# Kernel tuning notes

Hardware: AMD Instinct MI355X
Metric: run time of the kernel (lower is better)

The kernel has to match this reference:

```python
import jax, jax.numpy as jnp
import numpy as np

B, N, C = 16, 3136, 576
HEADS, AG, WIN, PS = 8, 49, 56, 7


def setup_inputs() -> dict:
    key = jax.random.key(0)
    ks = jax.random.split(key, 14)
    std = 0.02
    d = {
        "x": jax.random.normal(ks[0], (B, N, C), jnp.float32),
        "Wq": std * jax.random.normal(ks[1], (C, C), jnp.float32),
        "Wkv": std * jax.random.normal(ks[2], (C, 2 * C), jnp.float32),
        "an_bias": std * jax.random.normal(ks[3], (HEADS, AG, 7, 7), jnp.float32),
        "na_bias": std * jax.random.normal(ks[4], (HEADS, AG, 7, 7), jnp.float32),
        "ah_bias": std * jax.random.normal(ks[5], (1, HEADS, AG, WIN, 1), jnp.float32),
        "aw_bias": std * jax.random.normal(ks[6], (1, HEADS, AG, 1, WIN), jnp.float32),
        "ha_bias": std * jax.random.normal(ks[7], (1, HEADS, WIN, 1, AG), jnp.float32),
        "wa_bias": std * jax.random.normal(ks[8], (1, HEADS, 1, WIN, AG), jnp.float32),
        "dwc_w": std * jax.random.normal(ks[9], (C, 1, 3, 3), jnp.float32),  # depthwise 3x3
        "dwc_gamma": jnp.ones((C,), jnp.float32),
        "dwc_beta": jnp.zeros((C,), jnp.float32),
        "proj_w": std * jax.random.normal(ks[10], (C, C), jnp.float32),
        "proj_b": jnp.zeros((C,), jnp.float32),
        "H": 56,
        "W": 56,
    }
    return d


def _forward(x, Wq, Wkv, an_bias, na_bias, ah_bias, aw_bias, ha_bias, wa_bias,
             dwc_w, dwc_gamma, dwc_beta, proj_w, proj_b, H, W):
    b, n, c = x.shape
    heads, ag = an_bias.shape[0], an_bias.shape[1]
    hd = c // heads
    scale = hd ** -0.5

    q = x @ Wq                     # [b, n, c]
    kv = x @ Wkv                   # [b, n, 2c]
    k, v = kv[..., :c], kv[..., c:]

    # agent tokens: adaptive avg pool q (H,W grid) down to (PS, PS)
    ps = int(round(ag ** 0.5))
    qa = q.reshape(b, ps, H // ps, ps, W // ps, c).mean(axis=(2, 4))  # [b, ps, ps, c]
    a = qa.reshape(b, ag, heads, hd).transpose(0, 2, 1, 3)            # [b, h, ag, hd]

    qh = q.reshape(b, n, heads, hd).transpose(0, 2, 1, 3)  # [b, h, n, hd]
    kh = k.reshape(b, n, heads, hd).transpose(0, 2, 1, 3)
    vh = v.reshape(b, n, heads, hd).transpose(0, 2, 1, 3)

    # stage 1: agent attends to K/V, with interpolated + separable position bias
    pb1 = jax.image.resize(an_bias, (heads, ag, H, W), "linear").reshape(1, heads, ag, n)
    pb2 = (ah_bias + aw_bias).reshape(1, heads, ag, n)
    agent_scores = jnp.einsum("bhad,bhnd->bhan", a * scale, kh) + pb1 + pb2
    agent_attn = jax.nn.softmax(agent_scores, axis=-1)
    agent_v = jnp.einsum("bhan,bhnd->bhad", agent_attn, vh)  # [b, h, ag, hd]

    # stage 2: queries attend to agent tokens
    ab1 = jax.image.resize(na_bias, (heads, ag, H, W), "linear").reshape(1, heads, ag, n)
    ab1 = ab1.transpose(0, 1, 3, 2)                                   # [1, h, n, ag]
    ab2 = (ha_bias + wa_bias).reshape(1, heads, n, ag)
    q_scores = jnp.einsum("bhnd,bhad->bhna", qh * scale, a) + ab1 + ab2
    q_attn = jax.nn.softmax(q_scores, axis=-1)
    out = jnp.einsum("bhna,bhad->bhnd", q_attn, agent_v)
    out = out.transpose(0, 2, 1, 3).reshape(b, n, c)

    # depthwise-conv branch on v (DW_bn_relu, BN in eval mode with unit stats)
    vimg = v.transpose(0, 2, 1).reshape(b, c, H, W)
    y = jax.lax.conv_general_dilated(vimg, dwc_w, (1, 1), "SAME",
                                     feature_group_count=c,
                                     dimension_numbers=("NCHW", "OIHW", "NCHW"))
    y = jax.nn.relu(y * dwc_gamma[None, :, None, None] + dwc_beta[None, :, None, None])
    y = y.reshape(b, c, n).transpose(0, 2, 1)

    out = out + y
    out = out @ proj_w + proj_b   # output projection
    return out


def reference(x, Wq, Wkv, an_bias, na_bias, ah_bias, aw_bias, ha_bias, wa_bias,
              dwc_w, dwc_gamma, dwc_beta, proj_w, proj_b, H, W):
    return _forward(x, Wq, Wkv, an_bias, na_bias, ah_bias, aw_bias, ha_bias, wa_bias,
                    dwc_w, dwc_gamma, dwc_beta, proj_w, proj_b, H, W)
```

## Files before the change

kernel.cpp:

```cpp
#include <hip/hip_runtime.h>
#include <stdint.h>

typedef unsigned short u16;
typedef u16   u16x4 __attribute__((ext_vector_type(4)));
typedef u16   u16x8 __attribute__((ext_vector_type(8)));
typedef float f32x4 __attribute__((ext_vector_type(4)));
typedef __bf16 bf16x8 __attribute__((ext_vector_type(8)));

#define BB    16
#define NN    3136
#define CC    576
#define HEADS 8
#define HD    72
#define AGN   49
#define NTOT  1728
#define NCH   6
#define SCALE 0.1178511301977579f

__device__ __forceinline__ u16 f2bf(float f) {
    unsigned u = __float_as_uint(f);
    return (u16)((u + 0x7fffu + ((u >> 16) & 1u)) >> 16);
}
__device__ __forceinline__ float bf2f(u16 u) {
    return __uint_as_float(((unsigned)u) << 16);
}

__global__ __launch_bounds__(256) void k_cast_x(const float* __restrict__ x, u16* __restrict__ xb) {
    size_t i = (size_t)blockIdx.x * 256 + threadIdx.x;
    f32x4 v = *(const f32x4*)(x + i * 4);
    u16x4 o; o[0] = f2bf(v[0]); o[1] = f2bf(v[1]); o[2] = f2bf(v[2]); o[3] = f2bf(v[3]);
    *(u16x4*)(xb + i * 4) = o;
}

__global__ __launch_bounds__(256) void k_prep_w(const float* __restrict__ Wq, const float* __restrict__ Wkv,
                                                const float* __restrict__ Wp,
                                                u16* __restrict__ wbT, u16* __restrict__ wpT) {
    int idx = blockIdx.x * 256 + threadIdx.x;
    if (idx < NTOT * CC) {
        int nn = idx / CC, kk = idx % CC;
        float v = (nn < CC) ? Wq[kk * CC + nn] : Wkv[kk * (2 * CC) + (nn - CC)];
        wbT[idx] = f2bf(v);
    } else {
        int j = idx - NTOT * CC;
        int nn = j / CC, kk = j % CC;
        wpT[j] = f2bf(Wp[kk * CC + nn]);
    }
}

__device__ __forceinline__ float bilerp7(const float* __restrict__ g, int oy, int ox) {
    float cy = (oy - 3.5f) * 0.125f;
    float cx = (ox - 3.5f) * 0.125f;
    float fy0 = floorf(cy), fx0 = floorf(cx);
    float ty = cy - fy0, tx = cx - fx0;
    int iy0 = (int)fy0, ix0 = (int)fx0;
    int y0 = min(6, max(0, iy0)), y1 = min(6, max(0, iy0 + 1));
    int x0 = min(6, max(0, ix0)), x1 = min(6, max(0, ix0 + 1));
    float g00 = g[y0 * 7 + x0], g01 = g[y0 * 7 + x1];
    float g10 = g[y1 * 7 + x0], g11 = g[y1 * 7 + x1];
    return (1.f - ty) * ((1.f - tx) * g00 + tx * g01) + ty * ((1.f - tx) * g10 + tx * g11);
}

__global__ __launch_bounds__(256) void k_bias1(const float* __restrict__ an, const float* __restrict__ ah,
                                               const float* __restrict__ aw, float* __restrict__ b1) {
    int idx = blockIdx.x * 256 + threadIdx.x;
    int ag = idx % AGN; int r = idx / AGN; int n = r % NN; int h = r / NN;
    int y = n / 56, x = n % 56;
    float v = bilerp7(an + (h * AGN + ag) * 49, y, x);
    b1[idx] = v + ah[(h * AGN + ag) * 56 + y] + aw[(h * AGN + ag) * 56 + x];
}

__global__ __launch_bounds__(256) void k_bias2(const float* __restrict__ na, const float* __restrict__ ha,
                                               const float* __restrict__ wa, float* __restrict__ b2p) {
    int idx = blockIdx.x * 256 + threadIdx.x;
    int ag = idx & 63; int r = idx >> 6; int n = r % NN; int h = r / NN;
    float v;
    if (ag < AGN) {
        int y = n / 56, x = n % 56;
        v = bilerp7(na + (h * AGN + ag) * 49, y, x)
          + ha[(h * 56 + y) * AGN + ag] + wa[(h * 56 + x) * AGN + ag];
    } else v = -1e30f;
    b2p[idx] = v;
}

template<int MODE>
__global__ __launch_bounds__(256) void k_gemm(const u16* __restrict__ A, const u16* __restrict__ Bt,
                                              u16* __restrict__ Qp, u16* __restrict__ Kp, u16* __restrict__ Vp,
                                              float* __restrict__ Cf, const float* __restrict__ bias,
                                              const int M) {
    const int NB = (MODE == 0) ? NTOT : CC;
    __shared__ u16 SMEM[2 * 128 * 64];
    u16* Asm = SMEM;
    u16* Bsm = SMEM + 128 * 64;
    const int t = threadIdx.x, lane = t & 63, wid = t >> 6;
    const int wm = wid & 1, wn = wid >> 1;
    const int nwg = gridDim.x * gridDim.y;
    const int id = blockIdx.y * gridDim.x + blockIdx.x;
    const int qq = nwg >> 3, rr = nwg & 7;
    const int xcd = id & 7, off = id >> 3;
    const int nid = (xcd < rr ? xcd * (qq + 1) : rr * (qq + 1) + (xcd - rr) * qq) + off;
    const int row0 = (nid / gridDim.x) * 128, col0 = (nid % gridDim.x) * 128;
    const int lr = lane & 15, lk = lane >> 4;
    f32x4 acc[4][4];
#pragma unroll
    for (int m = 0; m < 4; m++)
#pragma unroll
        for (int n2 = 0; n2 < 4; n2++) acc[m][n2] = (f32x4)0.f;

    for (int kt = 0; kt < 9; ++kt) {
        const int k0 = kt * 64;
#pragma unroll
        for (int it = 0; it < 4; ++it) {
            int flat = it * 256 + wid * 64 + lane;
            int r = flat >> 3, lc = (flat & 7) ^ (r & 7);
            int arow = min(row0 + r, M - 1);
            const u16* src = A + (size_t)arow * CC + k0 + lc * 8;
            __builtin_amdgcn_global_load_lds((const __attribute__((address_space(1))) void*)src,
                                             (__attribute__((address_space(3))) void*)(&Asm[(it * 256 + wid * 64) * 8]),
                                             16, 0, 0);
        }
#pragma unroll
        for (int it = 0; it < 4; ++it) {
            int flat = it * 256 + wid * 64 + lane;
            int r = flat >> 3, lc = (flat & 7) ^ (r & 7);
            int brow = min(col0 + r, NB - 1);
            const u16* src = Bt + (size_t)brow * CC + k0 + lc * 8;
            __builtin_amdgcn_global_load_lds((const __attribute__((address_space(1))) void*)src,
                                             (__attribute__((address_space(3))) void*)(&Bsm[(it * 256 + wid * 64) * 8]),
                                             16, 0, 0);
        }
        __syncthreads();
#pragma unroll
        for (int kk = 0; kk < 2; ++kk) {
            const int klocal2 = (kk * 32 + lk * 8) * 2;
            bf16x8 av[4], bv[4];
#pragma unroll
            for (int m = 0; m < 4; m++) {
                int row = wm * 64 + m * 16 + lr;
                av[m] = *(const bf16x8*)((const char*)Asm + row * 128 + (klocal2 ^ ((row & 7) << 4)));
            }
#pragma unroll
            for (int n2 = 0; n2 < 4; n2++) {
                int row = wn * 64 + n2 * 16 + lr;
                bv[n2] = *(const bf16x8*)((const char*)Bsm + row * 128 + (klocal2 ^ ((row & 7) << 4)));
            }
#pragma unroll
            for (int m = 0; m < 4; m++)
#pragma unroll
                for (int n2 = 0; n2 < 4; n2++)
                    acc[m][n2] = __builtin_amdgcn_mfma_f32_16x16x32_bf16(av[m], bv[n2], acc[m][n2], 0, 0, 0);
        }
        __syncthreads();
    }

    if (MODE == 0) {
#pragma unroll
        for (int n2 = 0; n2 < 4; n2++) {
            int cgl = col0 + wn * 64 + n2 * 16 + lr;
            if (cgl >= NB) continue;
            int which = cgl / 576;
            int rem = cgl - which * 576;
            int hh = rem / 72;
            int dd = rem - hh * 72;
            u16* dst = which == 0 ? Qp : (which == 1 ? Kp : Vp);
#pragma unroll
            for (int m = 0; m < 4; m++)
#pragma unroll
                for (int j = 0; j < 4; j++) {
                    int rgl = row0 + wm * 64 + m * 16 + lk * 4 + j;
                    int b = rgl / NN, n = rgl - b * NN;
                    dst[((size_t)(b * 8 + hh) * NN + n) * 72 + dd] = f2bf(acc[m][n2][j]);
                }
        }
    } else {
        float* Ef = (float*)SMEM;
#pragma unroll
        for (int ph = 0; ph < 4; ++ph) {
            if (wm == (ph >> 1)) {
#pragma unroll
                for (int mm = 0; mm < 2; mm++) {
                    int m = (ph & 1) * 2 + mm;
#pragma unroll
                    for (int n2 = 0; n2 < 4; n2++) {
                        int col = wn * 64 + n2 * 16 + lr;
                        float addv = (MODE == 1) ? bias[min(col0 + col, NB - 1)] : 0.f;
#pragma unroll
                        for (int j = 0; j < 4; j++)
                            Ef[(mm * 16 + lk * 4 + j) * 136 + col] = acc[m][n2][j] + addv;
                    }
                }
            }
            __syncthreads();
#pragma unroll
            for (int cc2 = 0; cc2 < 4; ++cc2) {
                int cidx = cc2 * 256 + t;
                int rl = cidx >> 5, colc = cidx & 31;
                int cgl = col0 + colc * 4;
                int rgl = row0 + ph * 32 + rl;
                if (cgl < NB && rgl < M) {
                    f32x4 v = *(const f32x4*)&Ef[rl * 136 + colc * 4];
                    *(f32x4*)(Cf + (size_t)rgl * 576 + cgl) = v;
                }
            }
            __syncthreads();
        }
    }
}

__global__ __launch_bounds__(256) void k_poolx(const u16* __restrict__ xb, u16* __restrict__ px) {
    const int t = threadIdx.x;
    const int b = blockIdx.x / 7, p1 = blockIdx.x % 7;
    for (int task = t; task < 504; task += 256) {
        int p2 = task / 72, c8 = task - p2 * 72;
        const u16* base = xb + ((size_t)b * NN + (p1 * 8) * 56 + p2 * 8) * CC + c8 * 8;
        float s[8] = {0.f, 0.f, 0.f, 0.f, 0.f, 0.f, 0.f, 0.f};
        for (int y = 0; y < 8; ++y)
#pragma unroll
            for (int x = 0; x < 8; ++x) {
                u16x8 v = *(const u16x8*)(base + (size_t)(y * 56 + x) * CC);
#pragma unroll
                for (int j = 0; j < 8; j++) s[j] += bf2f(v[j]);
            }
        u16x8 o;
#pragma unroll
        for (int j = 0; j < 8; j++) o[j] = f2bf(s[j] * 0.015625f);
        *(u16x8*)(px + (size_t)(b * AGN + p1 * 7 + p2) * CC + c8 * 8) = o;
    }
}

__global__ __launch_bounds__(256) void k_stageA(const u16* __restrict__ Kp, const u16* __restrict__ Vp,
                                                const float* __restrict__ a_f, const float* __restrict__ b1,
                                                float* __restrict__ part) {
    const int t = threadIdx.x, lane = t & 63, w = t >> 6;
    const int c = lane & 15, g = lane >> 4;
    const int bh = blockIdx.y, b = bh >> 3, h = bh & 7;
    const int chunk = blockIdx.x;
    const int t0 = (chunk == 0) ? 0 : 9 + 8 * (chunk - 1);
    const int ntile = (chunk == 0) ? 9 : 8;

    __shared__ u16 A_lds[64][104];
    __shared__ u16 K_lds[64][104];
    __shared__ u16 Vt[80][72];
    __shared__ u16 P_lds[64][72];

    for (int i = t; i < 64 * 104; i += 256) {
        int r = i / 104, cc = i - r * 104;
        if (cc >= 72 || r >= 49) A_lds[r][cc] = 0;
        if (cc >= 72) K_lds[r][cc] = 0;
    }
    for (int i = t; i < 8 * 72; i += 256) Vt[72 + i / 72][i % 72] = 0;
    for (int i = t; i < 49 * 72; i += 256) {
        int r = i / 72, d = i - r * 72;
        A_lds[r][d] = f2bf(a_f[(size_t)(b * 49 + r) * CC + h * 72 + d] * SCALE);
    }
    __syncthreads();

    bf16x8 bfA[3];
#pragma unroll
    for (int ks = 0; ks < 3; ++ks) bfA[ks] = *(const bf16x8*)&A_lds[16 * w + c][8 * g + 32 * ks];

    float m_run = -1e30f, l_run = 0.f;
    f32x4 acc[5];
#pragma unroll
    for (int dt = 0; dt < 5; ++dt) acc[dt] = (f32x4)0.f;

    const u16* kb = Kp + ((size_t)(b * 8 + h) * NN + t0 * 64) * 72;
    const u16* vb = Vp + ((size_t)(b * 8 + h) * NN + t0 * 64) * 72;
    const int arow = min(16 * w + c, 48);

    for (int tile = 0; tile < ntile; ++tile) {
        for (int i = t; i < 576; i += 256) {
            int nl = i / 9, ch = i - nl * 9;
            u16x8 kd = *(const u16x8*)(kb + (size_t)tile * 4608 + i * 8);
            *(u16x8*)&K_lds[nl][ch * 8] = kd;
        }
        for (int i = t; i < 576; i += 256) {
            int ch = i >> 6, nl = i & 63;
            u16x8 vd = *(const u16x8*)(vb + (size_t)tile * 4608 + (nl * 9 + ch) * 8);
#pragma unroll
            for (int j = 0; j < 8; j++) Vt[ch * 8 + j][nl] = vd[j];
        }
        __syncthreads();

        f32x4 sT[4];
        const int nbase = (t0 + tile) * 64 + 4 * g;
#pragma unroll
        for (int nm = 0; nm < 4; ++nm) {
            f32x4 sv;
#pragma unroll
            for (int j = 0; j < 4; j++)
                sv[j] = b1[(size_t)(h * NN + nbase + 16 * nm + j) * AGN + arow];
#pragma unroll
            for (int ks = 0; ks < 3; ++ks) {
                bf16x8 af = *(const bf16x8*)&K_lds[16 * nm + c][8 * g + 32 * ks];
                sv = __builtin_amdgcn_mfma_f32_16x16x32_bf16(af, bfA[ks], sv, 0, 0, 0);
            }
            sT[nm] = sv;
        }

        float mt = sT[0][0];
#pragma unroll
        for (int nm = 0; nm < 4; ++nm)
#pragma unroll
            for (int j = 0; j < 4; j++) mt = fmaxf(mt, sT[nm][j]);
        mt = fmaxf(mt, __shfl_xor(mt, 16, 64));
        mt = fmaxf(mt, __shfl_xor(mt, 32, 64));
        float mnew = fmaxf(m_run, mt);
        float ps = 0.f;
#pragma unroll
        for (int nm = 0; nm < 4; ++nm) {
            float p0 = __expf(sT[nm][0] - mnew);
            float p1 = __expf(sT[nm][1] - mnew);
            float p2 = __expf(sT[nm][2] - mnew);
            float p3 = __expf(sT[nm][3] - mnew);
            ps += (p0 + p1) + (p2 + p3);
            unsigned pk01 = ((unsigned)f2bf(p1) << 16) | f2bf(p0);
            unsigned pk23 = ((unsigned)f2bf(p3) << 16) | f2bf(p2);
            unsigned* dst = (unsigned*)&P_lds[16 * w + c][16 * nm + 4 * g];
            dst[0] = pk01; dst[1] = pk23;
        }
        ps += __shfl_xor(ps, 16, 64);
        ps += __shfl_xor(ps, 32, 64);
        float rsc = __expf(m_run - mnew);
        l_run = l_run * rsc + ps;
        m_run = mnew;

        float rj[4];
#pragma unroll
        for (int j = 0; j < 4; j++) rj[j] = __shfl(rsc, 4 * g + j, 64);
        bf16x8 pa[2];
#pragma unroll
        for (int ks = 0; ks < 2; ++ks) pa[ks] = *(const bf16x8*)&P_lds[16 * w + c][8 * g + 32 * ks];
#pragma unroll
        for (int dt = 0; dt < 5; ++dt) {
            f32x4 a0 = acc[dt];
#pragma unroll
            for (int j = 0; j < 4; j++) a0[j] *= rj[j];
#pragma unroll
            for (int ks = 0; ks < 2; ++ks) {
                bf16x8 vf = *(const bf16x8*)&Vt[16 * dt + c][8 * g + 32 * ks];
                a0 = __builtin_amdgcn_mfma_f32_16x16x32_bf16(pa[ks], vf, a0, 0, 0, 0);
            }
            acc[dt] = a0;
        }
        __syncthreads();
    }

    const size_t pbase = (size_t)(bh * NCH + chunk) * (49 * 74);
#pragma unroll
    for (int dt = 0; dt < 5; ++dt) {
        int d = 16 * dt + c;
        if (d < 72) {
#pragma unroll
            for (int j = 0; j < 4; j++) {
                int agent = 16 * w + 4 * g + j;
                if (agent < 49) part[pbase + agent * 74 + d] = acc[dt][j];
            }
        }
    }
    if (g == 0) {
        int agent = 16 * w + c;
        if (agent < 49) {
            part[pbase + agent * 74 + 72] = m_run;
            part[pbase + agent * 74 + 73] = l_run;
        }
    }
}

__global__ __launch_bounds__(256) void k_reduceA(const float* __restrict__ part, float* __restrict__ agv) {
    const int bh = blockIdx.x, t = threadIdx.x;
    const float* pb = part + (size_t)bh * NCH * (49 * 74);
    for (int idx = t; idx < 49 * 72; idx += 256) {
        int row = idx / 72, d = idx - row * 72;
        float m = -1e30f;
#pragma unroll
        for (int c = 0; c < NCH; c++) m = fmaxf(m, pb[c * (49 * 74) + row * 74 + 72]);
        float accv = 0.f, l = 0.f;
#pragma unroll
        for (int c = 0; c < NCH; c++) {
            const float* pc = pb + c * (49 * 74) + row * 74;
            float e = __expf(pc[72] - m);
            accv += pc[d] * e;
            l += pc[73] * e;
        }
        agv[(size_t)(bh * 49 + row) * 72 + d] = accv / l;
    }
}

__global__ __launch_bounds__(256) void k_stageBC(const u16* __restrict__ Qp, const float* __restrict__ a_f,
                                                 const float* __restrict__ agv, const float* __restrict__ b2p,
                                                 const u16* __restrict__ Vp, const float* __restrict__ cw,
                                                 const float* __restrict__ gamma, const float* __restrict__ beta,
                                                 u16* __restrict__ pre) {
    const int t = threadIdx.x, lane = t & 63, w = t >> 6;
    const int c = lane & 15, g = lane >> 4;
    const int bh = blockIdx.y, b = bh >> 3, h = bh & 7;
    const int n0 = blockIdx.x * 256;

    __shared__ u16 A_lds[64][104];
    __shared__ u16 avT[80][72];
    __shared__ u16 Pt[4][64][80];
    __shared__ float wle[72 * 9];
    __shared__ float gle[72], ble[72];

    for (int i = t; i < 64 * 104; i += 256) {
        int r = i / 104, cc = i - r * 104;
        if (cc >= 72 || r >= 49) A_lds[r][cc] = 0;
    }
    for (int i = t; i < 80 * 72; i += 256) ((u16*)avT)[i] = 0;
    for (int i = t; i < 648; i += 256) wle[i] = cw[h * 648 + i];
    if (t < 72) { gle[t] = gamma[h * 72 + t]; ble[t] = beta[h * 72 + t]; }
    __syncthreads();
    for (int i = t; i < 49 * 72; i += 256) {
        int r = i / 72, d = i - r * 72;
        A_lds[r][d] = f2bf(a_f[(size_t)(b * 49 + r) * CC + h * 72 + d] * SCALE);
        avT[d][r]   = f2bf(agv[(size_t)(bh * 49 + r) * 72 + d]);
    }
    __syncthreads();

    bf16x8 afr[4][3];
#pragma unroll
    for (int mt = 0; mt < 4; ++mt)
#pragma unroll
        for (int ks = 0; ks < 3; ++ks) afr[mt][ks] = *(const bf16x8*)&A_lds[16 * mt + c][8 * g + 32 * ks];

    const int nw0 = n0 + w * 64;
#pragma unroll
    for (int cg = 0; cg < 4; ++cg) {
        const int n = nw0 + 16 * cg + c;
        const int ne = min(n, NN - 1);
        const u16* qp = Qp + ((size_t)(b * 8 + h) * NN + ne) * 72;
        bf16x8 qf[3];
#pragma unroll
        for (int ks = 0; ks < 3; ++ks) qf[ks] = *(const bf16x8*)(qp + 8 * g + 32 * ks);
        const float* bp = b2p + (size_t)(h * NN + ne) * 64;
        f32x4 sv[4];
#pragma unroll
        for (int mt = 0; mt < 4; ++mt) sv[mt] = *(const f32x4*)(bp + 16 * mt + 4 * g);
#pragma unroll
        for (int ks = 0; ks < 3; ++ks)
#pragma unroll
            for (int mt = 0; mt < 4; ++mt)
                sv[mt] = __builtin_amdgcn_mfma_f32_16x16x32_bf16(afr[mt][ks], qf[ks], sv[mt], 0, 0, 0);
        float mx = sv[0][0];
#pragma unroll
        for (int mt = 0; mt < 4; ++mt)
#pragma unroll
            for (int j = 0; j < 4; j++) mx = fmaxf(mx, sv[mt][j]);
        mx = fmaxf(mx, __shfl_xor(mx, 16, 64));
        mx = fmaxf(mx, __shfl_xor(mx, 32, 64));
        float ps = 0.f;
#pragma unroll
        for (int mt = 0; mt < 4; ++mt) {
#pragma unroll
            for (int j = 0; j < 4; j++) { sv[mt][j] = __expf(sv[mt][j] - mx); ps += sv[mt][j]; }
        }
        ps += __shfl_xor(ps, 16, 64);
        ps += __shfl_xor(ps, 32, 64);
        float inv = 1.f / ps;
#pragma unroll
        for (int mt = 0; mt < 4; ++mt) {
            unsigned pk01 = ((unsigned)f2bf(sv[mt][1] * inv) << 16) | f2bf(sv[mt][0] * inv);
            unsigned pk23 = ((unsigned)f2bf(sv[mt][3] * inv) << 16) | f2bf(sv[mt][2] * inv);
            unsigned* dst = (unsigned*)&Pt[w][16 * cg + c][16 * mt + 4 * g];
            dst[0] = pk01; dst[1] = pk23;
        }
    }
    bf16x8 vfr[5][2];
#pragma unroll
    for (int dt = 0; dt < 5; ++dt)
#pragma unroll
        for (int ks = 0; ks < 2; ++ks) vfr[dt][ks] = *(const bf16x8*)&avT[16 * dt + c][8 * g + 32 * ks];
#pragma unroll
    for (int rt = 0; rt < 4; ++rt) {
        bf16x8 pf[2];
#pragma unroll
        for (int ks = 0; ks < 2; ++ks) pf[ks] = *(const bf16x8*)&Pt[w][16 * rt + c][8 * g + 32 * ks];
#pragma unroll
        for (int dt = 0; dt < 5; ++dt) {
            f32x4 a0 = (f32x4)0.f;
            a0 = __builtin_amdgcn_mfma_f32_16x16x32_bf16(pf[0], vfr[dt][0], a0, 0, 0, 0);
            a0 = __builtin_amdgcn_mfma_f32_16x16x32_bf16(pf[1], vfr[dt][1], a0, 0, 0, 0);
            int dd = 16 * dt + c;
            if (dd < 72) {
#pragma unroll
                for (int j = 0; j < 4; j++)
                    Pt[w][16 * rt + 4 * g + j][dd] = f2bf(a0[j]);
            }
        }
    }
    __syncthreads();

    const u16* PtF = &Pt[0][0][0];
    const u16* vh = Vp + ((size_t)(b * 8 + h) * NN) * 72;
    for (int task = t; task < 256 * 9; task += 256) {
        int tl = task / 9, ch = task - tl * 9;
        int n = n0 + tl;
        if (n >= NN) continue;
        int y = n / 56, x = n % 56;
        float a[8] = {0.f, 0.f, 0.f, 0.f, 0.f, 0.f, 0.f, 0.f};
#pragma unroll
        for (int dy = -1; dy <= 1; ++dy) {
            int yy = y + dy; if (yy < 0 || yy > 55) continue;
#pragma unroll
            for (int dx = -1; dx <= 1; ++dx) {
                int xx = x + dx; if (xx < 0 || xx > 55) continue;
                u16x8 vv = *(const u16x8*)(vh + (size_t)(yy * 56 + xx) * 72 + ch * 8);
                int tap = (dy + 1) * 3 + (dx + 1);
#pragma unroll
                for (int j = 0; j < 8; j++) a[j] += bf2f(vv[j]) * wle[(ch * 8 + j) * 9 + tap];
            }
        }
        u16x8 ov = *(const u16x8*)&PtF[tl * 80 + ch * 8];
        u16x8 rr2;
#pragma unroll
        for (int j = 0; j < 8; j++)
            rr2[j] = f2bf(bf2f(ov[j]) + fmaxf(a[j] * gle[ch * 8 + j] + ble[ch * 8 + j], 0.f));
        *(u16x8*)(pre + ((size_t)b * NN + n) * CC + h * 72 + ch * 8) = rr2;
    }
}

extern "C" void kernel_launch(void* const* d_in, const int* in_sizes, int n_in,
                              void* d_out, int out_size, void* d_ws, size_t ws_size,
                              hipStream_t stream) {
    const float* x     = (const float*)d_in[0];
    const float* Wq    = (const float*)d_in[1];
    const float* Wkv   = (const float*)d_in[2];
    const float* an_b  = (const float*)d_in[3];
    const float* na_b  = (const float*)d_in[4];
    const float* ah_b  = (const float*)d_in[5];
    const float* aw_b  = (const float*)d_in[6];
    const float* ha_b  = (const float*)d_in[7];
    const float* wa_b  = (const float*)d_in[8];
    const float* dwcw  = (const float*)d_in[9];
    const float* gam   = (const float*)d_in[10];
    const float* bet   = (const float*)d_in[11];
    const float* projw = (const float*)d_in[12];
    const float* projb = (const float*)d_in[13];
    float* out = (float*)d_out;

    char* ws = (char*)d_ws;
    u16* wbT  = (u16*)(ws + 0);
    u16* wpT  = (u16*)(ws + 1990656);
    u16* xb   = (u16*)(ws + 2654208);
    u16* Qp   = (u16*)(ws + 60456960);
    u16* Kp   = (u16*)(ws + 118259712);
    u16* Vp   = (u16*)(ws + 176062464);
    float* af = (float*)(ws + 233865216);
    u16* px   = (u16*)(ws + 235671552);
    float* agv= (float*)(ws + 235671552);
    float* b1 = (float*)(ws + 237477888);
    float* b2p= (float*)(ws + 242395136);
    float* part = (float*)xb;

    k_cast_x<<<28224, 256, 0, stream>>>(x, xb);
    k_prep_w<<<5184, 256, 0, stream>>>(Wq, Wkv, projw, wbT, wpT);
    k_bias1<<<4802, 256, 0, stream>>>(an_b, ah_b, aw_b, b1);
    k_bias2<<<6272, 256, 0, stream>>>(na_b, ha_b, wa_b, b2p);
    k_poolx<<<112, 256, 0, stream>>>(xb, px);
    k_gemm<2><<<dim3(5, 7), 256, 0, stream>>>(px, wbT, nullptr, nullptr, nullptr, af, nullptr, 784);
    k_gemm<0><<<dim3(14, 392), 256, 0, stream>>>(xb, wbT, Qp, Kp, Vp, nullptr, nullptr, BB * NN);
    k_stageA<<<dim3(NCH, 128), 256, 0, stream>>>(Kp, Vp, af, b1, part);
    k_reduceA<<<128, 256, 0, stream>>>(part, agv);
    k_stageBC<<<dim3(13, 128), 256, 0, stream>>>(Qp, af, agv, b2p, Vp, dwcw, gam, bet, xb );
    k_gemm<1><<<dim3(5, 392), 256, 0, stream>>>(xb , wpT, nullptr, nullptr, nullptr, out, projb, BB * NN);
}
```

Before: 487.7 us.

## Precompute scaled agent and transposed agent-V bf16 tiles outside stageBC

Result: faster. 442.0 us (-9.4%).

```diff
diff --git a/kernel.cpp b/kernel.cpp
--- a/kernel.cpp
+++ b/kernel.cpp
@@ -227,6 +227,15 @@
     }
 }
 
+__global__ __launch_bounds__(256) void k_prepA(const float* __restrict__ a_f, u16* __restrict__ aSc) {
+    int idx = blockIdx.x * 256 + threadIdx.x;
+    int d = idx % 96; int r = (idx / 96) & 63; int bh = idx / (96 * 64);
+    int b = bh >> 3, h = bh & 7;
+    u16 v = 0;
+    if (r < AGN && d < HD) v = f2bf(a_f[((size_t)b * AGN + r) * CC + h * HD + d] * SCALE);
+    aSc[idx] = v;
+}
+
 __global__ __launch_bounds__(256) void k_stageA(const u16* __restrict__ Kp, const u16* __restrict__ Vp,
                                                 const float* __restrict__ a_f, const float* __restrict__ b1,
                                                 float* __restrict__ part) {
@@ -366,9 +375,12 @@
     }
 }
 
-__global__ __launch_bounds__(256) void k_reduceA(const float* __restrict__ part, float* __restrict__ agv) {
+__global__ __launch_bounds__(256) void k_reduceA(const float* __restrict__ part, u16* __restrict__ avTg) {
     const int bh = blockIdx.x, t = threadIdx.x;
     const float* pb = part + (size_t)bh * NCH * (49 * 74);
+    u16* av = avTg + (size_t)bh * 80 * 72;
+    for (int i = t; i < 80 * 72; i += 256) av[i] = 0;
+    __syncthreads();
     for (int idx = t; idx < 49 * 72; idx += 256) {
         int row = idx / 72, d = idx - row * 72;
         float m = -1e30f;
@@ -382,12 +394,12 @@
             accv += pc[d] * e;
             l += pc[73] * e;
         }
-        agv[(size_t)(bh * 49 + row) * 72 + d] = accv / l;
-    }
-}
-
-__global__ __launch_bounds__(256) void k_stageBC(const u16* __restrict__ Qp, const float* __restrict__ a_f,
-                                                 const float* __restrict__ agv, const float* __restrict__ b2p,
+        av[d * 72 + row] = f2bf(accv / l);
+    }
+}
+
+__global__ __launch_bounds__(256) void k_stageBC(const u16* __restrict__ Qp, const u16* __restrict__ aSc,
+                                                 const u16* __restrict__ avTg, const float* __restrict__ b2p,
                                                  const u16* __restrict__ Vp, const float* __restrict__ cw,
                                                  const float* __restrict__ gamma, const float* __restrict__ beta,
                                                  u16* __restrict__ pre) {
@@ -396,32 +408,25 @@
     const int bh = blockIdx.y, b = bh >> 3, h = bh & 7;
     const int n0 = blockIdx.x * 256;
 
-    __shared__ u16 A_lds[64][104];
-    __shared__ u16 avT[80][72];
-    __shared__ u16 Pt[4][64][80];
+    __shared__ u16 Pt[4][64][88];
     __shared__ float wle[72 * 9];
     __shared__ float gle[72], ble[72];
 
-    for (int i = t; i < 64 * 104; i += 256) {
-        int r = i / 104, cc = i - r * 104;
-        if (cc >= 72 || r >= 49) A_lds[r][cc] = 0;
-    }
-    for (int i = t; i < 80 * 72; i += 256) ((u16*)avT)[i] = 0;
     for (int i = t; i < 648; i += 256) wle[i] = cw[h * 648 + i];
     if (t < 72) { gle[t] = gamma[h * 72 + t]; ble[t] = beta[h * 72 + t]; }
-    __syncthreads();
-    for (int i = t; i < 49 * 72; i += 256) {
-        int r = i / 72, d = i - r * 72;
-        A_lds[r][d] = f2bf(a_f[(size_t)(b * 49 + r) * CC + h * 72 + d] * SCALE);
-        avT[d][r]   = f2bf(agv[(size_t)(bh * 49 + r) * 72 + d]);
-    }
-    __syncthreads();
-
+
+    const u16* aB = aSc + (size_t)bh * 64 * 96;
     bf16x8 afr[4][3];
 #pragma unroll
     for (int mt = 0; mt < 4; ++mt)
 #pragma unroll
-        for (int ks = 0; ks < 3; ++ks) afr[mt][ks] = *(const bf16x8*)&A_lds[16 * mt + c][8 * g + 32 * ks];
+        for (int ks = 0; ks < 3; ++ks) afr[mt][ks] = *(const bf16x8*)(aB + (16 * mt + c) * 96 + 8 * g + 32 * ks);
+    const u16* vB = avTg + (size_t)bh * 80 * 72;
+    bf16x8 vfr[5][2];
+#pragma unroll
+    for (int dt = 0; dt < 5; ++dt)
+#pragma unroll
+        for (int ks = 0; ks < 2; ++ks) vfr[dt][ks] = *(const bf16x8*)(vB + (16 * dt + c) * 72 + 8 * g + 32 * ks);
 
     const int nw0 = n0 + w * 64;
 #pragma unroll
@@ -465,11 +470,6 @@
             dst[0] = pk01; dst[1] = pk23;
         }
     }
-    bf16x8 vfr[5][2];
-#pragma unroll
-    for (int dt = 0; dt < 5; ++dt)
-#pragma unroll
-        for (int ks = 0; ks < 2; ++ks) vfr[dt][ks] = *(const bf16x8*)&avT[16 * dt + c][8 * g + 32 * ks];
 #pragma unroll
     for (int rt = 0; rt < 4; ++rt) {
         bf16x8 pf[2];
@@ -478,13 +478,12 @@
 #pragma unroll
         for (int dt = 0; dt < 5; ++dt) {
             f32x4 a0 = (f32x4)0.f;
-            a0 = __builtin_amdgcn_mfma_f32_16x16x32_bf16(pf[0], vfr[dt][0], a0, 0, 0, 0);
-            a0 = __builtin_amdgcn_mfma_f32_16x16x32_bf16(pf[1], vfr[dt][1], a0, 0, 0, 0);
-            int dd = 16 * dt + c;
-            if (dd < 72) {
-#pragma unroll
-                for (int j = 0; j < 4; j++)
-                    Pt[w][16 * rt + 4 * g + j][dd] = f2bf(a0[j]);
+            a0 = __builtin_amdgcn_mfma_f32_16x16x32_bf16(vfr[dt][0], pf[0], a0, 0, 0, 0);
+            a0 = __builtin_amdgcn_mfma_f32_16x16x32_bf16(vfr[dt][1], pf[1], a0, 0, 0, 0);
+            int d0 = 16 * dt + 4 * g;
+            if (d0 < 72) {
+                u16x4 rr; rr[0] = f2bf(a0[0]); rr[1] = f2bf(a0[1]); rr[2] = f2bf(a0[2]); rr[3] = f2bf(a0[3]);
+                *(u16x4*)&Pt[w][16 * rt + c][d0] = rr;
             }
         }
     }
@@ -510,7 +509,7 @@
                 for (int j = 0; j < 8; j++) a[j] += bf2f(vv[j]) * wle[(ch * 8 + j) * 9 + tap];
             }
         }
-        u16x8 ov = *(const u16x8*)&PtF[tl * 80 + ch * 8];
+        u16x8 ov = *(const u16x8*)&PtF[tl * 88 + ch * 8];
         u16x8 rr2;
 #pragma unroll
         for (int j = 0; j < 8; j++)
@@ -547,10 +546,11 @@
     u16* Vp   = (u16*)(ws + 176062464);
     float* af = (float*)(ws + 233865216);
     u16* px   = (u16*)(ws + 235671552);
-    float* agv= (float*)(ws + 235671552);
+    u16* avTg = (u16*)(ws + 235671552);
     float* b1 = (float*)(ws + 237477888);
     float* b2p= (float*)(ws + 242395136);
     float* part = (float*)xb;
+    u16* aSc = Kp;
 
     k_cast_x<<<28224, 256, 0, stream>>>(x, xb);
     k_prep_w<<<5184, 256, 0, stream>>>(Wq, Wkv, projw, wbT, wpT);
@@ -560,7 +560,8 @@
     k_gemm<2><<<dim3(5, 7), 256, 0, stream>>>(px, wbT, nullptr, nullptr, nullptr, af, nullptr, 784);
     k_gemm<0><<<dim3(14, 392), 256, 0, stream>>>(xb, wbT, Qp, Kp, Vp, nullptr, nullptr, BB * NN);
     k_stageA<<<dim3(NCH, 128), 256, 0, stream>>>(Kp, Vp, af, b1, part);
-    k_reduceA<<<128, 256, 0, stream>>>(part, agv);
-    k_stageBC<<<dim3(13, 128), 256, 0, stream>>>(Qp, af, agv, b2p, Vp, dwcw, gam, bet, xb );
+    k_reduceA<<<128, 256, 0, stream>>>(part, avTg);
+    k_prepA<<<3072, 256, 0, stream>>>(af, aSc);
+    k_stageBC<<<dim3(13, 128), 256, 0, stream>>>(Qp, aSc, avTg, b2p, Vp, dwcw, gam, bet, xb );
     k_gemm<1><<<dim3(5, 392), 256, 0, stream>>>(xb , wpT, nullptr, nullptr, nullptr, out, projb, BB * NN);
 }
```
